# Kernel optimization log

Hardware: AMD Instinct MI355X
Metric: run time of the kernel (lower is better)

The kernel has to match this reference:

```python
import jax, jax.numpy as jnp
import numpy as np

NUM_CLASSES = 80
ROI_SIZE = 7
SAMPLING = 2          # RoIAlign sampling_ratio
STRIDES = (4, 8, 16, 32)
FINEST_SCALE = 56.0
SCORE_THR = 0.05
IOU_THR = 0.5
MAX_PER_IMG = 100
MEANS = jnp.zeros((4,), jnp.float32)
STDS = jnp.array([0.1, 0.1, 0.2, 0.2], jnp.float32)
MAX_RATIO = abs(float(np.log(16.0 / 1000.0)))


def setup_inputs() -> dict:
    key = jax.random.key(0)
    ks = jax.random.split(key, 20)
    C, H0, W0 = 256, 200, 336
    inp = {}
    for i in range(4):
        inp[f"feat{i}"] = jax.random.normal(ks[i], (1, C, H0 >> i, W0 >> i), jnp.float32)
    N = 1000
    IMG_W, IMG_H = 1344.0, 800.0
    cx = jax.random.uniform(ks[4], (N,), minval=0.0, maxval=IMG_W)
    cy = jax.random.uniform(ks[5], (N,), minval=0.0, maxval=IMG_H)
    w = jax.random.uniform(ks[6], (N,), minval=16.0, maxval=512.0)
    h = jax.random.uniform(ks[7], (N,), minval=16.0, maxval=512.0)
    x1 = jnp.clip(cx - w / 2, 0.0, IMG_W - 1)
    y1 = jnp.clip(cy - h / 2, 0.0, IMG_H - 1)
    x2 = jnp.clip(cx + w / 2, x1 + 1.0, IMG_W)
    y2 = jnp.clip(cy + h / 2, y1 + 1.0, IMG_H)
    inp["proposals"] = jnp.stack([x1, y1, x2, y2], axis=-1)
    D = C * ROI_SIZE * ROI_SIZE  # 12544
    FC = 1024
    inp["fc1_w"] = 0.01 * jax.random.normal(ks[8], (FC, D), jnp.float32)
    inp["fc1_b"] = jnp.zeros((FC,), jnp.float32)
    inp["fc2_w"] = 0.01 * jax.random.normal(ks[9], (FC, FC), jnp.float32)
    inp["fc2_b"] = jnp.zeros((FC,), jnp.float32)
    inp["cls_w"] = 0.01 * jax.random.normal(ks[10], (NUM_CLASSES + 1, FC), jnp.float32)
    inp["cls_b"] = jnp.zeros((NUM_CLASSES + 1,), jnp.float32)
    inp["reg_w"] = 0.01 * jax.random.normal(ks[11], (NUM_CLASSES * 4, FC), jnp.float32)
    inp["reg_b"] = jnp.zeros((NUM_CLASSES * 4,), jnp.float32)
    return inp


def _roi_align(feat, rois, scale):
    # feat [C,H,W]; rois [N,4]; aligned RoIAlign, 7x7 out, sampling_ratio=2
    C, H, W = feat.shape
    P = ROI_SIZE * SAMPLING  # 14 uniform sample points per axis

    def one(roi):
        x1, y1, x2, y2 = roi[0], roi[1], roi[2], roi[3]
        sx = x1 * scale - 0.5
        sy = y1 * scale - 0.5
        rw = (x2 - x1) * scale
        rh = (y2 - y1) * scale
        pts = (jnp.arange(P, dtype=feat.dtype) + 0.5) / P
        xs = sx + pts * rw
        ys = sy + pts * rh
        y0 = jnp.floor(ys)
        x0 = jnp.floor(xs)
        ly = ys - y0
        lx = xs - x0
        y0i = jnp.clip(y0.astype(jnp.int32), 0, H - 1)
        y1i = jnp.clip(y0i + 1, 0, H - 1)
        x0i = jnp.clip(x0.astype(jnp.int32), 0, W - 1)
        x1i = jnp.clip(x0i + 1, 0, W - 1)
        g = lambda yi, xi: feat[:, yi[:, None], xi[None, :]]  # [C,P,P]
        ly_ = ly[None, :, None]
        lx_ = lx[None, None, :]
        val = (1 - ly_) * ((1 - lx_) * g(y0i, x0i) + lx_ * g(y0i, x1i)) \
            + ly_ * ((1 - lx_) * g(y1i, x0i) + lx_ * g(y1i, x1i))
        vy = ((ys >= -1.0) & (ys <= H))[None, :, None]
        vx = ((xs >= -1.0) & (xs <= W))[None, None, :]
        val = jnp.where(vy & vx, val, 0.0)
        # average-pool the 2x2 samples per bin -> [C,7,7]
        return val.reshape(C, ROI_SIZE, SAMPLING, ROI_SIZE, SAMPLING).mean(axis=(2, 4))

    return jax.vmap(one)(rois)  # [N,C,7,7]


def _delta2bbox(proposals, deltas):
    d = deltas.reshape(-1, NUM_CLASSES, 4) * STDS + MEANS
    dx, dy = d[..., 0], d[..., 1]
    dw = jnp.clip(d[..., 2], -MAX_RATIO, MAX_RATIO)
    dh = jnp.clip(d[..., 3], -MAX_RATIO, MAX_RATIO)
    px = ((proposals[:, 0] + proposals[:, 2]) * 0.5)[:, None]
    py = ((proposals[:, 1] + proposals[:, 3]) * 0.5)[:, None]
    pw = (proposals[:, 2] - proposals[:, 0])[:, None]
    ph = (proposals[:, 3] - proposals[:, 1])[:, None]
    gw = pw * jnp.exp(dw)
    gh = ph * jnp.exp(dh)
    gx = px + pw * dx
    gy = py + ph * dy
    return jnp.stack([gx - gw * 0.5, gy - gh * 0.5, gx + gw * 0.5, gy + gh * 0.5], axis=-1)


def _pairwise_iou(b):
    x1, y1, x2, y2 = b[:, 0], b[:, 1], b[:, 2], b[:, 3]
    area = jnp.maximum(x2 - x1, 0.0) * jnp.maximum(y2 - y1, 0.0)
    iw = jnp.maximum(jnp.minimum(x2[:, None], x2[None, :]) - jnp.maximum(x1[:, None], x1[None, :]), 0.0)
    ih = jnp.maximum(jnp.minimum(y2[:, None], y2[None, :]) - jnp.maximum(y1[:, None], y1[None, :]), 0.0)
    inter = iw * ih
    return inter / jnp.maximum(area[:, None] + area[None, :] - inter, 1e-8)


def _nms_one_class(boxes, scores):
    # greedy NMS, static shapes; returns score-sorted boxes/scores + keep mask
    N = scores.shape[0]
    order = jnp.argsort(-scores)
    b = boxes[order]
    s = scores[order]
    iou = _pairwise_iou(b)
    idx = jnp.arange(N)

    def body(i, keep):
        sup = (iou[i] > IOU_THR) & keep[i] & (idx > i)
        return keep & jnp.logical_not(sup)

    keep = jax.lax.fori_loop(0, N, body, s > SCORE_THR)
    return b, s, keep


def _batched_nms(bboxes, scores):
    # bboxes [N,81,4], scores [N,81]; class 80 is background (skipped)
    cls_boxes = jnp.transpose(bboxes[:, :NUM_CLASSES, :], (1, 0, 2))  # [80,N,4]
    cls_scores = scores[:, :NUM_CLASSES].T                            # [80,N]
    b, s, keep = jax.vmap(_nms_one_class)(cls_boxes, cls_scores)
    N = s.shape[1]
    s_flat = jnp.where(keep, s, -1.0).reshape(-1)
    topv, topi = jax.lax.top_k(s_flat, MAX_PER_IMG)
    det_boxes = b.reshape(-1, 4)[topi]
    det_classes = (topi // N).astype(jnp.int32)
    valid = topv > 0.0
    num_det = valid.sum().astype(jnp.int32)
    det_scores = jnp.where(valid, topv, 0.0)
    det_boxes = jnp.where(valid[:, None], det_boxes, 0.0)
    det_classes = jnp.where(valid, det_classes, -1)
    return num_det, det_boxes[None], det_scores[None], det_classes[None]


def _forward(feat0, feat1, feat2, feat3, proposals,
             fc1_w, fc1_b, fc2_w, fc2_b, cls_w, cls_b, reg_w, reg_b):
    feats = [feat0[0], feat1[0], feat2[0], feat3[0]]
    wp = proposals[:, 2] - proposals[:, 0]
    hp = proposals[:, 3] - proposals[:, 1]
    scale = jnp.sqrt(jnp.maximum(wp * hp, 1e-6))
    lvl = jnp.clip(jnp.floor(jnp.log2(scale / FINEST_SCALE + 1e-6)), 0, 3).astype(jnp.int32)
    N = proposals.shape[0]
    C = feats[0].shape[0]
    roi_feats = jnp.zeros((N, C, ROI_SIZE, ROI_SIZE), proposals.dtype)
    for l, stride in enumerate(STRIDES):
        f = _roi_align(feats[l], proposals, 1.0 / stride)
        roi_feats = jnp.where((lvl == l)[:, None, None, None], f, roi_feats)
    h = roi_feats.reshape(N, -1)
    h = jax.nn.relu(h @ fc1_w.T + fc1_b)
    h = jax.nn.relu(h @ fc2_w.T + fc2_b)
    cls_score = h @ cls_w.T + cls_b          # [N,81]
    bbox_pred = h @ reg_w.T + reg_b          # [N,320]
    scores = jax.nn.softmax(cls_score, axis=1)
    boxes = _delta2bbox(proposals, bbox_pred)                          # [N,80,4]
    boxes = jnp.concatenate([boxes, jnp.zeros((N, 1, 4), boxes.dtype)], axis=1)
    return _batched_nms(boxes, scores)


def reference(feat0, feat1, feat2, feat3, proposals,
              fc1_w, fc1_b, fc2_w, fc2_b, cls_w, cls_b, reg_w, reg_b):
    return _forward(feat0, feat1, feat2, feat3, proposals,
                    fc1_w, fc1_b, fc2_w, fc2_b, cls_w, cls_b, reg_w, reg_b)
```

## Files before the change

### kernel.cpp

```cpp
#include <hip/hip_runtime.h>
#include <math.h>

#define NCLS   80
#define NPROP  1000
#define FCDIM  1024
#define DFLAT  12544
#define MPAD   1024
#define MAXR   4.1351665567423560f
#define LDSP   40
#define NMSW   16
#define NCAT   404

#define CSPLIT 8
#define CG     (256 / CSPLIT)

typedef unsigned short ushort_t;
typedef unsigned long long ull_t;
using short8  = __attribute__((ext_vector_type(8))) short;
using float4v = __attribute__((ext_vector_type(4))) float;

__device__ inline ushort_t f2bf(float f) {
    unsigned int u = __float_as_uint(f);
    unsigned int r = (u + 0x7fffu + ((u >> 16) & 1u)) >> 16;
    return (ushort_t)r;
}

__device__ __forceinline__ unsigned cvtpk_bf16(float lo, float hi) {
    unsigned r;
    asm("v_cvt_pk_bf16_f32 %0, %1, %2" : "=v"(r) : "v"(lo), "v"(hi));
    return r;
}

__global__ __launch_bounds__(256) void roi_align_k(
    const float* __restrict__ f0, const float* __restrict__ f1,
    const float* __restrict__ f2, const float* __restrict__ f3,
    const float* __restrict__ props, ushort_t* __restrict__ Abf)
{
    int r  = blockIdx.x;
    int cz = blockIdx.y;
    int t  = threadIdx.x;

    if (r >= NPROP) {
        for (int i = t; i < CG * 49; i += 256)
            Abf[(size_t)r * DFLAT + cz * (CG * 49) + i] = 0;
        return;
    }

    const float4 p = *(const float4*)&props[(size_t)r * 4];
    float wp = p.z - p.x, hp = p.w - p.y;
    float scale = sqrtf(fmaxf(wp * hp, 1e-6f));
    int lvl = (int)floorf(log2f(scale / 56.0f + 1e-6f));
    lvl = min(max(lvl, 0), 3);

    const float* f; int H, W; float sc;
    switch (lvl) {
        case 0:  f = f0; H = 200; W = 336; sc = 0.25f;    break;
        case 1:  f = f1; H = 100; W = 168; sc = 0.125f;   break;
        case 2:  f = f2; H = 50;  W = 84;  sc = 0.0625f;  break;
        default: f = f3; H = 25;  W = 42;  sc = 0.03125f; break;
    }

    if (t >= 196) return;

    int b   = t >> 2;
    int sub = t & 3;
    int by = b / 7, bx = b - by * 7;
    int sy = by * 2 + (sub >> 1);
    int sx = bx * 2 + (sub & 1);

    float startx = p.x * sc - 0.5f, rangex = (p.z - p.x) * sc;
    float starty = p.y * sc - 0.5f, rangey = (p.w - p.y) * sc;
    float posx = startx + (((float)sx + 0.5f) / 14.0f) * rangex;
    float posy = starty + (((float)sy + 0.5f) / 14.0f) * rangey;

    float flx = floorf(posx), fly = floorf(posy);
    float lx = posx - flx, ly = posy - fly;
    int x0 = min(max((int)flx, 0), W - 1);
    int y0 = min(max((int)fly, 0), H - 1);
    int y1 = min(y0 + 1, H - 1);
    bool valid = (posx >= -1.0f) && (posx <= (float)W) &&
                 (posy >= -1.0f) && (posy <= (float)H);
    float vm = valid ? 0.25f : 0.0f;

    float w00 = (1.f - ly) * (1.f - lx) * vm;
    float w01 = (1.f - ly) * lx * vm;
    float w10 = ly * (1.f - lx) * vm;
    float w11 = ly * lx * vm;

    int  xb = min(x0, W - 2);
    bool xr = (x0 == W - 1);
    float wtA = xr ? 0.f : w00, wtB = xr ? (w00 + w01) : w01;
    float wbA = xr ? 0.f : w10, wbB = xr ? (w10 + w11) : w11;
    int ot = y0 * W + xb;
    int ob = y1 * W + xb;

    const int HW = H * W;
    ushort_t* orow = Abf + (size_t)r * DFLAT + cz * (CG * 49);
    const float* pl = f + (size_t)(cz * CG) * HW;

    #pragma unroll 8
    for (int c = 0; c < CG; c++) {
        float2 tv = *(const float2*)(pl + ot);
        float2 bv = *(const float2*)(pl + ob);
        float v = tv.x * wtA + tv.y * wtB + bv.x * wbA + bv.y * wbB;
        v += __shfl_xor(v, 1);
        v += __shfl_xor(v, 2);
        if (sub == 0)
            orow[c * 49 + b] = f2bf(v);
        pl += HW;
    }
}

__global__ __launch_bounds__(256) void gemm_sk_k(
    const ushort_t* __restrict__ A, const float* __restrict__ Wf,
    float* __restrict__ P, int N, int K, int KC)
{
    __shared__ ushort_t As[2][128 * LDSP];
    __shared__ ushort_t Bs[2][128 * LDSP];

    int tid = threadIdx.x;
    int w = tid >> 6, l = tid & 63;
    int wm = (w >> 1) * 64, wn = (w & 1) * 64;

    int bid = (int)blockIdx.x + (int)gridDim.x * ((int)blockIdx.y + (int)gridDim.y * (int)blockIdx.z);
    int bx = bid & 7;
    int slot = bid >> 3;
    int by = slot % (int)gridDim.y;
    int bz = slot / (int)gridDim.y;

    int m0 = by * 128, n0 = bx * 128;
    int kc0 = bz * KC;

    int lrow = tid >> 2;
    int lko  = (tid & 3) * 8;

    const ushort_t* Ag = A  + (size_t)(m0 + lrow) * K + kc0 + lko;
    const float*    Wg = Wf + (size_t)(n0 + lrow) * K + kc0 + lko;
    size_t rowK64 = (size_t)64 * K;

    float4v acc[4][4];
    #pragma unroll
    for (int i = 0; i < 4; i++)
        #pragma unroll
        for (int j = 0; j < 4; j++)
            acc[i][j] = (float4v){0.f, 0.f, 0.f, 0.f};

    int rl = l & 15, q = l >> 4;

    {
        uint4  a0  = *(const uint4*)(Ag);
        uint4  a1  = *(const uint4*)(Ag + rowK64);
        float4 w0a = *(const float4*)(Wg);
        float4 w0b = *(const float4*)(Wg + 4);
        float4 w1a = *(const float4*)(Wg + rowK64);
        float4 w1b = *(const float4*)(Wg + rowK64 + 4);
        uint4 wv0, wv1;
        wv0.x = cvtpk_bf16(w0a.x, w0a.y); wv0.y = cvtpk_bf16(w0a.z, w0a.w);
        wv0.z = cvtpk_bf16(w0b.x, w0b.y); wv0.w = cvtpk_bf16(w0b.z, w0b.w);
        wv1.x = cvtpk_bf16(w1a.x, w1a.y); wv1.y = cvtpk_bf16(w1a.z, w1a.w);
        wv1.z = cvtpk_bf16(w1b.x, w1b.y); wv1.w = cvtpk_bf16(w1b.z, w1b.w);
        *(uint4*)&As[0][lrow * LDSP + lko]        = a0;
        *(uint4*)&As[0][(lrow + 64) * LDSP + lko] = a1;
        *(uint4*)&Bs[0][lrow * LDSP + lko]        = wv0;
        *(uint4*)&Bs[0][(lrow + 64) * LDSP + lko] = wv1;
    }
    __syncthreads();

    int cur = 0;
    for (int k0 = 0; k0 < KC; k0 += 32) {
        bool more = (k0 + 32) < KC;

        uint4 na0, na1;
        float4 nw0a, nw0b, nw1a, nw1b;
        if (more) {
            na0  = *(const uint4*)(Ag + k0 + 32);
            na1  = *(const uint4*)(Ag + rowK64 + k0 + 32);
            nw0a = *(const float4*)(Wg + k0 + 32);
            nw0b = *(const float4*)(Wg + k0 + 36);
            nw1a = *(const float4*)(Wg + rowK64 + k0 + 32);
            nw1b = *(const float4*)(Wg + rowK64 + k0 + 36);
        }

        const ushort_t* Ac = As[cur];
        const ushort_t* Bc = Bs[cur];
        short8 af[4], bfr[4];
        #pragma unroll
        for (int i = 0; i < 4; i++)
            af[i] = *(const short8*)&Ac[(wm + i * 16 + rl) * LDSP + q * 8];
        #pragma unroll
        for (int j = 0; j < 4; j++)
            bfr[j] = *(const short8*)&Bc[(wn + j * 16 + rl) * LDSP + q * 8];

        #pragma unroll
        for (int i = 0; i < 4; i++)
            #pragma unroll
            for (int j = 0; j < 4; j++)
                acc[i][j] = __builtin_amdgcn_mfma_f32_16x16x32_bf16(
                    af[i], bfr[j], acc[i][j], 0, 0, 0);

        if (more) {
            uint4 wv0, wv1;
            wv0.x = cvtpk_bf16(nw0a.x, nw0a.y); wv0.y = cvtpk_bf16(nw0a.z, nw0a.w);
            wv0.z = cvtpk_bf16(nw0b.x, nw0b.y); wv0.w = cvtpk_bf16(nw0b.z, nw0b.w);
            wv1.x = cvtpk_bf16(nw1a.x, nw1a.y); wv1.y = cvtpk_bf16(nw1a.z, nw1a.w);
            wv1.z = cvtpk_bf16(nw1b.x, nw1b.y); wv1.w = cvtpk_bf16(nw1b.z, nw1b.w);
            ushort_t* An = As[cur ^ 1];
            ushort_t* Bn = Bs[cur ^ 1];
            *(uint4*)&An[lrow * LDSP + lko]        = na0;
            *(uint4*)&An[(lrow + 64) * LDSP + lko] = na1;
            *(uint4*)&Bn[lrow * LDSP + lko]        = wv0;
            *(uint4*)&Bn[(lrow + 64) * LDSP + lko] = wv1;
        }

        __syncthreads();
        cur ^= 1;
    }

    float* Pz = P + (size_t)bz * ((size_t)MPAD * N);
    #pragma unroll
    for (int i = 0; i < 4; i++) {
        #pragma unroll
        for (int j = 0; j < 4; j++) {
            int col = n0 + wn + j * 16 + rl;
            #pragma unroll
            for (int rr = 0; rr < 4; rr++) {
                int row = m0 + wm + i * 16 + q * 4 + rr;
                Pz[(size_t)row * N + col] = acc[i][j][rr];
            }
        }
    }
}

__global__ __launch_bounds__(256) void reduce_sk_k(
    const float* __restrict__ P, const float* __restrict__ bias,
    void* __restrict__ Cout, int N, int SK, int relu, int out_bf16)
{
    size_t idx = ((size_t)blockIdx.x * 256 + threadIdx.x) * 4;
    float4 s = *(const float4*)&P[idx];
    for (int z = 1; z < SK; z++) {
        float4 pv = *(const float4*)&P[(size_t)z * ((size_t)MPAD * N) + idx];
        s.x += pv.x; s.y += pv.y; s.z += pv.z; s.w += pv.w;
    }
    int n = (int)(idx % N);
    float4 b = *(const float4*)&bias[n];
    s.x += b.x; s.y += b.y; s.z += b.z; s.w += b.w;
    if (relu) {
        s.x = fmaxf(s.x, 0.f); s.y = fmaxf(s.y, 0.f);
        s.z = fmaxf(s.z, 0.f); s.w = fmaxf(s.w, 0.f);
    }
    if (out_bf16) {
        ushort4 o;
        o.x = f2bf(s.x); o.y = f2bf(s.y); o.z = f2bf(s.z); o.w = f2bf(s.w);
        *(ushort4*)&((ushort_t*)Cout)[idx] = o;
    } else {
        *(float4*)&((float*)Cout)[idx] = s;
    }
}

__global__ __launch_bounds__(256) void concat_w_k(
    const float* __restrict__ reg_w, const float* __restrict__ cls_w,
    const float* __restrict__ reg_b, const float* __restrict__ cls_b,
    float* __restrict__ Wcat, float* __restrict__ bcat)
{
    int row = blockIdx.x;
    int t = threadIdx.x;
    float4 v = make_float4(0.f, 0.f, 0.f, 0.f);
    float bv = 0.f;
    if (row < 320) {
        v = *(const float4*)&reg_w[(size_t)row * FCDIM + t * 4];
        bv = reg_b[row];
    } else if (row < NCAT - 3) {
        v = *(const float4*)&cls_w[(size_t)(row - 320) * FCDIM + t * 4];
        bv = cls_b[row - 320];
    }
    *(float4*)&Wcat[(size_t)row * FCDIM + t * 4] = v;
    if (t == 0) bcat[row] = bv;
}

__global__ __launch_bounds__(256) void gemm_tn_k(
    const float* __restrict__ A, const float* __restrict__ W,
    const float* __restrict__ bias, float* __restrict__ C,
    int M, int N, int K, int relu)
{
    __shared__ float As[16][64];
    __shared__ float Bs[16][64];

    int tid = threadIdx.x;
    int tx = tid & 15;
    int ty = tid >> 4;
    int m0 = blockIdx.y * 64, n0 = blockIdx.x * 64;

    int lr = tid >> 2;
    int lk = (tid & 3) << 2;

    const float* Arow = A + (size_t)(m0 + lr) * K + lk;
    const float* Wrow = W + (size_t)(n0 + lr) * K + lk;
    bool mOK = (m0 + lr) < M;
    bool nOK = (n0 + lr) < N;

    float acc[4][4] = {};

    for (int k0 = 0; k0 < K; k0 += 16) {
        float4 av = mOK ? *(const float4*)(Arow + k0) : make_float4(0.f, 0.f, 0.f, 0.f);
        float4 wv = nOK ? *(const float4*)(Wrow + k0) : make_float4(0.f, 0.f, 0.f, 0.f);
        As[lk + 0][lr] = av.x; As[lk + 1][lr] = av.y;
        As[lk + 2][lr] = av.z; As[lk + 3][lr] = av.w;
        Bs[lk + 0][lr] = wv.x; Bs[lk + 1][lr] = wv.y;
        Bs[lk + 2][lr] = wv.z; Bs[lk + 3][lr] = wv.w;
        __syncthreads();

        #pragma unroll
        for (int kk = 0; kk < 16; kk++) {
            float4 a = *(const float4*)&As[kk][ty << 2];
            float4 b = *(const float4*)&Bs[kk][tx << 2];
            acc[0][0] += a.x * b.x; acc[0][1] += a.x * b.y;
            acc[0][2] += a.x * b.z; acc[0][3] += a.x * b.w;
            acc[1][0] += a.y * b.x; acc[1][1] += a.y * b.y;
            acc[1][2] += a.y * b.z; acc[1][3] += a.y * b.w;
            acc[2][0] += a.z * b.x; acc[2][1] += a.z * b.y;
            acc[2][2] += a.z * b.z; acc[2][3] += a.z * b.w;
            acc[3][0] += a.w * b.x; acc[3][1] += a.w * b.y;
            acc[3][2] += a.w * b.z; acc[3][3] += a.w * b.w;
        }
        __syncthreads();
    }

    #pragma unroll
    for (int i = 0; i < 4; i++) {
        int m = m0 + (ty << 2) + i;
        if (m >= M) continue;
        #pragma unroll
        for (int j = 0; j < 4; j++) {
            int n = n0 + (tx << 2) + j;
            if (n < N) {
                float v = acc[i][j] + bias[n];
                if (relu) v = fmaxf(v, 0.f);
                C[(size_t)m * N + n] = v;
            }
        }
    }
}

__global__ __launch_bounds__(128) void head_post_k(
    const float* __restrict__ hr_s, const float* __restrict__ props,
    float* __restrict__ probsT, float* __restrict__ boxesT)
{
    int r = blockIdx.x, t = threadIdx.x;
    __shared__ float red[128];

    float x = (t < 81) ? hr_s[(size_t)r * NCAT + 320 + t] : -1e30f;
    red[t] = x; __syncthreads();
    for (int s = 64; s > 0; s >>= 1) {
        if (t < s) red[t] = fmaxf(red[t], red[t + s]);
        __syncthreads();
    }
    float mx = red[0];
    __syncthreads();

    float e = (t < 81) ? expf(x - mx) : 0.f;
    red[t] = e; __syncthreads();
    for (int s = 64; s > 0; s >>= 1) {
        if (t < s) red[t] += red[t + s];
        __syncthreads();
    }
    float inv = 1.f / red[0];

    if (t < NCLS) {
        probsT[(size_t)t * NPROP + r] = e * inv;

        const float4 p = *(const float4*)&props[(size_t)r * 4];
        float4 d = *(const float4*)&hr_s[(size_t)r * NCAT + t * 4];
        float dx = d.x * 0.1f, dy = d.y * 0.1f;
        float dw = fminf(fmaxf(d.z * 0.2f, -MAXR), MAXR);
        float dh = fminf(fmaxf(d.w * 0.2f, -MAXR), MAXR);
        float px = (p.x + p.z) * 0.5f, py = (p.y + p.w) * 0.5f;
        float pw = p.z - p.x, ph = p.w - p.y;
        float gw = pw * expf(dw), gh = ph * expf(dh);
        float gx = px + pw * dx, gy = py + ph * dy;
        float4 bo = make_float4(gx - gw * 0.5f, gy - gh * 0.5f,
                                gx + gw * 0.5f, gy + gh * 0.5f);
        *(float4*)&boxesT[(size_t)(t * NPROP + r) * 4] = bo;
    }
}

__global__ __launch_bounds__(512) void sort_k(
    const float* __restrict__ probsT, const float* __restrict__ boxesT,
    float* __restrict__ sortedS, float* __restrict__ sortedB)
{
    int c = blockIdx.x, t = threadIdx.x;
    __shared__ float sk[1024];
    __shared__ int   si[1024];

    for (int j = t; j < 1024; j += 512) {
        sk[j] = (j < NPROP) ? probsT[(size_t)c * NPROP + j] : -1e30f;
        si[j] = j;
    }
    __syncthreads();

    for (int size = 2; size <= 1024; size <<= 1) {
        for (int stride = size >> 1; stride > 0; stride >>= 1) {
            int i = (t << 1) - (t & (stride - 1));
            int j = i + stride;
            float ka = sk[i], kb = sk[j];
            int ia = si[i], ib = si[j];
            bool aFirst = (ka > kb) || (ka == kb && ia < ib);
            bool desc = ((i & size) == 0);
            if (desc ? !aFirst : aFirst) {
                sk[i] = kb; sk[j] = ka; si[i] = ib; si[j] = ia;
            }
            __syncthreads();
        }
    }

    for (int j = t; j < NPROP; j += 512) {
        sortedS[(size_t)c * NPROP + j] = sk[j];
        const float4 bb = *(const float4*)&boxesT[(size_t)(c * NPROP + si[j]) * 4];
        *(float4*)&sortedB[(size_t)(c * NPROP + j) * 4] = bb;
    }
}

__global__ __launch_bounds__(256) void nms_k(
    const float* __restrict__ sortedS, const float* __restrict__ sortedB,
    ull_t* __restrict__ masks, float* __restrict__ candS, int* __restrict__ candI)
{
    int c = blockIdx.x, t = threadIdx.x;
    __shared__ float x1s[NPROP], y1s[NPROP], x2s[NPROP], y2s[NPROP], ars[NPROP];
    __shared__ unsigned char kp[NPROP];
    __shared__ int segc[256];

    for (int j = t; j < NPROP; j += 256) {
        float4 b = *(const float4*)&sortedB[(size_t)(c * NPROP + j) * 4];
        x1s[j] = b.x; y1s[j] = b.y; x2s[j] = b.z; y2s[j] = b.w;
        ars[j] = fmaxf(b.z - b.x, 0.f) * fmaxf(b.w - b.y, 0.f);
        kp[j] = sortedS[(size_t)c * NPROP + j] > 0.05f ? 1 : 0;
    }
    __syncthreads();

    ull_t* M = masks + (size_t)c * NPROP * NMSW;
    for (int i = t; i < NPROP; i += 256) {
        if (!kp[i]) continue;
        float xi1 = x1s[i], yi1 = y1s[i], xi2 = x2s[i], yi2 = y2s[i], ai = ars[i];
        for (int w = 0; w < NMSW; w++) {
            ull_t m = 0ull;
            int j0 = w << 6;
            #pragma unroll 4
            for (int k = 0; k < 64; k++) {
                int j = j0 + k;
                if (j < NPROP) {
                    float iw = fmaxf(fminf(xi2, x2s[j]) - fmaxf(xi1, x1s[j]), 0.f);
                    float ih = fmaxf(fminf(yi2, y2s[j]) - fmaxf(yi1, y1s[j]), 0.f);
                    float inter = iw * ih;
                    float iou = inter / fmaxf(ai + ars[j] - inter, 1e-8f);
                    if (iou > 0.5f) m |= (1ull << k);
                }
            }
            M[(size_t)i * NMSW + w] = m;
        }
    }
    __syncthreads();

    if (t < 64) {
        ull_t rem = 0ull;
        for (int i = 0; i < NPROP; i++) {
            if (kp[i]) {
                ull_t w = __shfl(rem, i >> 6);
                if ((w >> (i & 63)) & 1ull) {
                    if (t == 0) kp[i] = 0;
                } else {
                    if (t < NMSW) rem |= M[(size_t)i * NMSW + t];
                }
            }
        }
    }
    __syncthreads();

    int j0 = t * 4;
    int cnt = 0;
    #pragma unroll
    for (int k = 0; k < 4; k++) {
        int j = j0 + k;
        if (j < NPROP && kp[j]) cnt++;
    }
    segc[t] = cnt;
    __syncthreads();
    for (int off = 1; off < 256; off <<= 1) {
        int add = (t >= off) ? segc[t - off] : 0;
        __syncthreads();
        segc[t] += add;
        __syncthreads();
    }
    int pos = segc[t] - cnt;
    #pragma unroll
    for (int k = 0; k < 4; k++) {
        int j = j0 + k;
        if (j < NPROP && kp[j]) {
            if (pos < 100) {
                candS[c * 100 + pos] = sortedS[(size_t)c * NPROP + j];
                candI[c * 100 + pos] = c * NPROP + j;
            }
            pos++;
        }
    }
    int total = segc[255];
    for (int p = total + t; p < 100; p += 256) {
        candS[c * 100 + p] = -2e30f;
        candI[c * 100 + p] = 0x7fffffff;
    }
}

__global__ __launch_bounds__(256) void merge_k(
    const float* __restrict__ candS, const int* __restrict__ candI,
    const float* __restrict__ sortedB, float* __restrict__ out)
{
    int t = threadIdx.x;
    __shared__ float cs[NCLS * 101];
    __shared__ int   ci[NCLS * 101];
    __shared__ float topv[100];
    __shared__ int   topi[100];

    for (int i = t; i < NCLS * 100; i += 256) {
        int c = i / 100, j = i - c * 100;
        cs[c * 101 + j] = candS[i];
        ci[c * 101 + j] = candI[i];
    }
    __syncthreads();

    if (t < 64) {
        int h1 = 0, h2 = 0;
        int c2 = t + 64;
        for (int r = 0; r < 100; r++) {
            float v = -2e30f; int fi = 0x7fffffff; int cls = 0;
            if (h1 < 100) { v = cs[t * 101 + h1]; fi = ci[t * 101 + h1]; cls = t; }
            if (c2 < NCLS && h2 < 100) {
                float v2 = cs[c2 * 101 + h2]; int fi2 = ci[c2 * 101 + h2];
                if (v2 > v || (v2 == v && fi2 < fi)) { v = v2; fi = fi2; cls = c2; }
            }
            #pragma unroll
            for (int s = 1; s < 64; s <<= 1) {
                float ov = __shfl_xor(v, s);
                int ofi  = __shfl_xor(fi, s);
                int ocl  = __shfl_xor(cls, s);
                if (ov > v || (ov == v && ofi < fi)) { v = ov; fi = ofi; cls = ocl; }
            }
            if (t == 0) { topv[r] = v; topi[r] = fi; }
            if (cls == t) h1++;
            else if (c2 < NCLS && cls == c2) h2++;
        }
    }
    __syncthreads();

    if (t < 100) {
        float v = topv[t]; int fi = topi[t];
        bool valid = v > 0.0f;
        float4 bb = make_float4(0.f, 0.f, 0.f, 0.f);
        if (valid) bb = *(const float4*)&sortedB[(size_t)fi * 4];
        out[1 + t * 4 + 0] = bb.x;
        out[1 + t * 4 + 1] = bb.y;
        out[1 + t * 4 + 2] = bb.z;
        out[1 + t * 4 + 3] = bb.w;
        out[401 + t] = valid ? v : 0.0f;
        out[501 + t] = valid ? (float)(fi / NPROP) : -1.0f;
    }
    if (t == 0) {
        int n = 0;
        for (int r = 0; r < 100; r++) n += (topv[r] > 0.0f) ? 1 : 0;
        out[0] = (float)n;
    }
}

extern "C" void kernel_launch(void* const* d_in, const int* in_sizes, int n_in,
                              void* d_out, int out_size, void* d_ws, size_t ws_size,
                              hipStream_t stream)
{
    const float* f0    = (const float*)d_in[0];
    const float* f1    = (const float*)d_in[1];
    const float* f2    = (const float*)d_in[2];
    const float* f3    = (const float*)d_in[3];
    const float* props = (const float*)d_in[4];
    const float* fc1_w = (const float*)d_in[5];
    const float* fc1_b = (const float*)d_in[6];
    const float* fc2_w = (const float*)d_in[7];
    const float* fc2_b = (const float*)d_in[8];
    const float* cls_w = (const float*)d_in[9];
    const float* cls_b = (const float*)d_in[10];
    const float* reg_w = (const float*)d_in[11];
    const float* reg_b = (const float*)d_in[12];
    float* out = (float*)d_out;

    unsigned char* base = (unsigned char*)d_ws;
    ushort_t* Abf  = (ushort_t*)(base);
    ushort_t* h1   = (ushort_t*)(base + 25690112);
    float*    P1   = (float*)(base + 27787264);
    float*    P2   = (float*)(base + 27787264);
    float*    h2   = (float*)(base + 44564480);
    float*    hr_s    = (float*)(base + 48758784);
    float*    probsT  = (float*)(base + 50401280);
    float*    boxesT  = (float*)(base + 50721280);
    float*    sortedS = (float*)(base + 52001280);
    float*    sortedB = (float*)(base + 52321280);
    float*    candS   = (float*)(base + 53601280);
    int*      candI   = (int*)(base + 53633280);
    float*    Wcat    = (float*)(base + 53665280);
    float*    bcat    = (float*)(base + 55320064);
    ull_t*    masks   = (ull_t*)(base);

    roi_align_k<<<dim3(MPAD, CSPLIT), 256, 0, stream>>>(f0, f1, f2, f3, props, Abf);

    gemm_sk_k<<<dim3(FCDIM / 128, MPAD / 128, 8), 256, 0, stream>>>(
        Abf, fc1_w, P1, FCDIM, DFLAT, DFLAT / 8);
    reduce_sk_k<<<(MPAD * FCDIM / 4) / 256, 256, 0, stream>>>(
        P1, fc1_b, h1, FCDIM, 8, 1, 1);

    concat_w_k<<<NCAT, 256, 0, stream>>>(reg_w, cls_w, reg_b, cls_b, Wcat, bcat);

    gemm_sk_k<<<dim3(FCDIM / 128, MPAD / 128, 4), 256, 0, stream>>>(
        h1, fc2_w, P2, FCDIM, FCDIM, FCDIM / 4);
    reduce_sk_k<<<(MPAD * FCDIM / 4) / 256, 256, 0, stream>>>(
        P2, fc2_b, h2, FCDIM, 4, 1, 0);

    gemm_tn_k<<<dim3((NCAT + 63) / 64, (NPROP + 63) / 64), 256, 0, stream>>>(
        h2, Wcat, bcat, hr_s, NPROP, NCAT, FCDIM, 0);

    head_post_k<<<NPROP, 128, 0, stream>>>(hr_s, props, probsT, boxesT);
    sort_k<<<NCLS, 512, 0, stream>>>(probsT, boxesT, sortedS, sortedB);
    nms_k<<<NCLS, 256, 0, stream>>>(sortedS, sortedB, masks, candS, candI);
    merge_k<<<1, 256, 0, stream>>>(candS, candI, sortedB, out);
}
```

Measured before the change: 544.9 us.

## Store split-K partials in bf16 and raise split-K factors for FC GEMMs

After: 558.8 us. 1.03x slower.

```diff
diff --git a/kernel.cpp b/kernel.cpp
--- a/kernel.cpp
+++ b/kernel.cpp
@@ -10,6 +10,8 @@
 #define LDSP   40
 #define NMSW   16
 #define NCAT   404
+#define SK1    14
+#define SK2    8
 
 #define CSPLIT 8
 #define CG     (256 / CSPLIT)
@@ -23,6 +25,9 @@
     unsigned int u = __float_as_uint(f);
     unsigned int r = (u + 0x7fffu + ((u >> 16) & 1u)) >> 16;
     return (ushort_t)r;
+}
+__device__ inline float bf2f(ushort_t u) {
+    return __uint_as_float(((unsigned int)u) << 16);
 }
 
 __device__ __forceinline__ unsigned cvtpk_bf16(float lo, float hi) {
@@ -113,7 +118,7 @@
 
 __global__ __launch_bounds__(256) void gemm_sk_k(
     const ushort_t* __restrict__ A, const float* __restrict__ Wf,
-    float* __restrict__ P, int N, int K, int KC)
+    ushort_t* __restrict__ P, int N, int K, int KC)
 {
     __shared__ ushort_t As[2][128 * LDSP];
     __shared__ ushort_t Bs[2][128 * LDSP];
@@ -216,7 +221,7 @@
         cur ^= 1;
     }
 
-    float* Pz = P + (size_t)bz * ((size_t)MPAD * N);
+    ushort_t* Pz = P + (size_t)bz * ((size_t)MPAD * N);
     #pragma unroll
     for (int i = 0; i < 4; i++) {
         #pragma unroll
@@ -225,21 +230,22 @@
             #pragma unroll
             for (int rr = 0; rr < 4; rr++) {
                 int row = m0 + wm + i * 16 + q * 4 + rr;
-                Pz[(size_t)row * N + col] = acc[i][j][rr];
-            }
-        }
-    }
-}
-
-__global__ __launch_bounds__(256) void reduce_sk_k(
-    const float* __restrict__ P, const float* __restrict__ bias,
+                Pz[(size_t)row * N + col] = f2bf(acc[i][j][rr]);
+            }
+        }
+    }
+}
+
+__global__ __launch_bounds__(256) void reduce_bf_k(
+    const ushort_t* __restrict__ P, const float* __restrict__ bias,
     void* __restrict__ Cout, int N, int SK, int relu, int out_bf16)
 {
     size_t idx = ((size_t)blockIdx.x * 256 + threadIdx.x) * 4;
-    float4 s = *(const float4*)&P[idx];
-    for (int z = 1; z < SK; z++) {
-        float4 pv = *(const float4*)&P[(size_t)z * ((size_t)MPAD * N) + idx];
-        s.x += pv.x; s.y += pv.y; s.z += pv.z; s.w += pv.w;
+    float4 s = make_float4(0.f, 0.f, 0.f, 0.f);
+    for (int z = 0; z < SK; z++) {
+        ushort4 pv = *(const ushort4*)&P[(size_t)z * ((size_t)MPAD * N) + idx];
+        s.x += bf2f(pv.x); s.y += bf2f(pv.y);
+        s.z += bf2f(pv.z); s.w += bf2f(pv.w);
     }
     int n = (int)(idx % N);
     float4 b = *(const float4*)&bias[n];
@@ -518,10 +524,14 @@
     __shared__ float topv[100];
     __shared__ int   topi[100];
 
-    for (int i = t; i < NCLS * 100; i += 256) {
-        int c = i / 100, j = i - c * 100;
-        cs[c * 101 + j] = candS[i];
-        ci[c * 101 + j] = candI[i];
+    {
+        int wv = t >> 6, ln = t & 63;
+        for (int c = wv; c < NCLS; c += 4) {
+            for (int j = ln; j < 100; j += 64) {
+                cs[c * 101 + j] = candS[c * 100 + j];
+                ci[c * 101 + j] = candI[c * 100 + j];
+            }
+        }
     }
     __syncthreads();
 
@@ -590,8 +600,8 @@
     unsigned char* base = (unsigned char*)d_ws;
     ushort_t* Abf  = (ushort_t*)(base);
     ushort_t* h1   = (ushort_t*)(base + 25690112);
-    float*    P1   = (float*)(base + 27787264);
-    float*    P2   = (float*)(base + 27787264);
+    ushort_t* P1b  = (ushort_t*)(base + 27787264);
+    ushort_t* P2b  = (ushort_t*)(base + 27787264);
     float*    h2   = (float*)(base + 44564480);
     float*    hr_s    = (float*)(base + 48758784);
     float*    probsT  = (float*)(base + 50401280);
@@ -606,17 +616,17 @@
 
     roi_align_k<<<dim3(MPAD, CSPLIT), 256, 0, stream>>>(f0, f1, f2, f3, props, Abf);
 
-    gemm_sk_k<<<dim3(FCDIM / 128, MPAD / 128, 8), 256, 0, stream>>>(
-        Abf, fc1_w, P1, FCDIM, DFLAT, DFLAT / 8);
-    reduce_sk_k<<<(MPAD * FCDIM / 4) / 256, 256, 0, stream>>>(
-        P1, fc1_b, h1, FCDIM, 8, 1, 1);
+    gemm_sk_k<<<dim3(FCDIM / 128, MPAD / 128, SK1), 256, 0, stream>>>(
+        Abf, fc1_w, P1b, FCDIM, DFLAT, DFLAT / SK1);
+    reduce_bf_k<<<(MPAD * FCDIM / 4) / 256, 256, 0, stream>>>(
+        P1b, fc1_b, h1, FCDIM, SK1, 1, 1);
 
     concat_w_k<<<NCAT, 256, 0, stream>>>(reg_w, cls_w, reg_b, cls_b, Wcat, bcat);
 
-    gemm_sk_k<<<dim3(FCDIM / 128, MPAD / 128, 4), 256, 0, stream>>>(
-        h1, fc2_w, P2, FCDIM, FCDIM, FCDIM / 4);
-    reduce_sk_k<<<(MPAD * FCDIM / 4) / 256, 256, 0, stream>>>(
-        P2, fc2_b, h2, FCDIM, 4, 1, 0);
+    gemm_sk_k<<<dim3(FCDIM / 128, MPAD / 128, SK2), 256, 0, stream>>>(
+        h1, fc2_w, P2b, FCDIM, FCDIM, FCDIM / SK2);
+    reduce_bf_k<<<(MPAD * FCDIM / 4) / 256, 256, 0, stream>>>(
+        P2b, fc2_b, h2, FCDIM, SK2, 1, 0);
 
     gemm_tn_k<<<dim3((NCAT + 63) / 64, (NPROP + 63) / 64), 256, 0, stream>>>(
         h2, Wcat, bcat, hr_s, NPROP, NCAT, FCDIM, 0);
```
